# Performance work log

Hardware: AMD Instinct MI355X
Metric: run time of the kernel (lower is better)

Reference implementation:

```python
import jax, jax.numpy as jnp
import numpy as np

B, S, H, NH = 2, 2048, 1024, 16
D = H // NH


def setup_inputs() -> dict:
    key = jax.random.key(0)
    ks = jax.random.split(key, 7)
    scale = 1.0 / np.sqrt(H)
    return {
        "x": jax.random.normal(ks[0], (B, S, H), dtype=jnp.float32),
        "Wq": jax.random.normal(ks[1], (H, H), dtype=jnp.float32) * scale,
        "bq": jax.random.normal(ks[2], (H,), dtype=jnp.float32) * 0.01,
        "Wk": jax.random.normal(ks[3], (H, H), dtype=jnp.float32) * scale,
        "bk": jax.random.normal(ks[4], (H,), dtype=jnp.float32) * 0.01,
        "Wv": jax.random.normal(ks[5], (H, H), dtype=jnp.float32) * scale,
        "bv": jax.random.normal(ks[6], (H,), dtype=jnp.float32) * 0.01,
    }


def reference(x, Wq, bq, Wk, bk, Wv, bv):
    b, s, h = x.shape
    n, d = NH, h // NH
    # QKV projections (torch Linear: x @ W.T + b)
    q = (x @ Wq.T + bq).reshape(b, s, n, d).transpose(0, 2, 1, 3)  # [b,n,s,d]
    k = (x @ Wk.T + bk).reshape(b, s, n, d).transpose(0, 2, 1, 3)
    v = (x @ Wv.T + bv).reshape(b, s, n, d).transpose(0, 2, 1, 3)
    # NOTE: original module applies NO 1/sqrt(d) scaling -- stay faithful.
    scores = jnp.einsum("bnqd,bnkd->bnqk", q, k)  # [b,n,s,s]
    probs = jax.nn.softmax(scores, axis=-1)
    attn = jnp.einsum("bnqk,bnkd->bnqd", probs, v)  # [b,n,s,d]
    return attn.transpose(0, 2, 1, 3).reshape(b, s, h)
```

## Files before the change

kernel.cpp:

```cpp
#include <hip/hip_runtime.h>
#include <hip/hip_bf16.h>

typedef unsigned int uint;
typedef unsigned short ushort;
typedef _Float16 f16;
typedef __attribute__((ext_vector_type(4))) float f32x4;
typedef __attribute__((ext_vector_type(8))) _Float16 f16x8;
typedef __attribute__((ext_vector_type(8))) ushort ushort8;

#define MFMAH(a, b, c) __builtin_amdgcn_mfma_f32_16x16x32_f16((a), (b), (c), 0, 0, 0)

#if __has_builtin(__builtin_amdgcn_permlane32_swap) && __has_builtin(__builtin_amdgcn_permlane16_swap)
#define HAVE_PERMLANE_SWAP 1
#else
#define HAVE_PERMLANE_SWAP 0
#endif

__device__ __forceinline__ ushort f2h(float x) {
    f16 h = (f16)x;
    return __builtin_bit_cast(ushort, h);
}
__device__ __forceinline__ uint pk_f16(float lo, float hi) {
    auto t = __builtin_amdgcn_cvt_pkrtz(lo, hi);
    return __builtin_bit_cast(uint, t);
}

__device__ __forceinline__ void gload_lds16(const void* g, void* l) {
    __builtin_amdgcn_global_load_lds(
        (const __attribute__((address_space(1))) void*)g,
        (__attribute__((address_space(3))) void*)l, 16, 0, 0);
}

__global__ __launch_bounds__(256) void cvt_all(const float* __restrict__ x,
                                               const float* __restrict__ Wq,
                                               const float* __restrict__ Wk,
                                               const float* __restrict__ Wv,
                                               ushort* __restrict__ xf,
                                               ushort* __restrict__ wf) {
    const int blk = blockIdx.x;
    const float* src;
    ushort* dst;
    int i;
    if (blk < 2048) {
        src = x;  dst = xf;              i = blk * 256 + threadIdx.x;
    } else if (blk < 2560) {
        src = Wq; dst = wf;              i = (blk - 2048) * 256 + threadIdx.x;
    } else if (blk < 3072) {
        src = Wk; dst = wf + 1024 * 1024; i = (blk - 2560) * 256 + threadIdx.x;
    } else {
        src = Wv; dst = wf + 2 * 1024 * 1024; i = (blk - 3072) * 256 + threadIdx.x;
    }
    const float4* s4 = reinterpret_cast<const float4*>(src);
    float4 a = s4[2 * i], b = s4[2 * i + 1];
    float v[8] = {a.x, a.y, a.z, a.w, b.x, b.y, b.z, b.w};
    ushort8 o;
#pragma unroll
    for (int j = 0; j < 8; ++j) o[j] = f2h(v[j]);
    *reinterpret_cast<ushort8*>(dst + i * 8) = o;
}

__global__ __launch_bounds__(256, 3) void qkv_gemm(const ushort* __restrict__ xf,
                                                   const ushort* __restrict__ wf,
                                                   const float* __restrict__ bq,
                                                   const float* __restrict__ bk,
                                                   const float* __restrict__ bv,
                                                   ushort* __restrict__ qh,
                                                   ushort* __restrict__ kh,
                                                   ushort* __restrict__ vt) {
    __shared__ ushort Asf[128 * 64];
    __shared__ ushort Bsf[128 * 64];
    const int tid = threadIdx.x;
    const int l = tid & 63, w = tid >> 6;
    const int lrow = l & 15, lhi = l >> 4;
    const int wr = w >> 1, wc = w & 1;
    const int m0 = blockIdx.x * 128;
    const int n0 = blockIdx.y * 128;
    const int z = blockIdx.z;
    const ushort* wz = wf + z * (1024 * 1024);
    const float* bias = (z == 0) ? bq : (z == 1) ? bk : bv;

    f32x4 acc[4][4] = {};
    const int srow = w * 32 + (l >> 3);
    const int scol = ((l & 7) ^ (l >> 3)) * 8;
    const int lds0 = w * 2048;
    const int arow = wr * 64 + lrow;
    const int brow = wc * 64 + lrow;

    for (int kt = 0; kt < 16; ++kt) {
        const int kb = kt * 64;
#pragma unroll
        for (int i = 0; i < 4; ++i) {
            gload_lds16(xf + (m0 + srow + i * 8) * 1024 + kb + scol, &Asf[lds0 + i * 512]);
            gload_lds16(wz + (n0 + srow + i * 8) * 1024 + kb + scol, &Bsf[lds0 + i * 512]);
        }
        __syncthreads();
#pragma unroll
        for (int kk = 0; kk < 2; ++kk) {
            const int csw = ((kk * 4 + lhi) ^ (lrow & 7)) * 8;
            f16x8 axf[4];
#pragma unroll
            for (int mi = 0; mi < 4; ++mi)
                axf[mi] = *reinterpret_cast<const f16x8*>(&Asf[(arow + mi * 16) * 64 + csw]);
            __builtin_amdgcn_s_setprio(1);
#pragma unroll
            for (int ni = 0; ni < 4; ++ni) {
                f16x8 bf8 = *reinterpret_cast<const f16x8*>(&Bsf[(brow + ni * 16) * 64 + csw]);
#pragma unroll
                for (int mi = 0; mi < 4; ++mi)
                    acc[mi][ni] = MFMAH(axf[mi], bf8, acc[mi][ni]);
            }
            __builtin_amdgcn_s_setprio(0);
        }
        __syncthreads();
    }
    float bcol[4];
#pragma unroll
    for (int ni = 0; ni < 4; ++ni) bcol[ni] = bias[n0 + wc * 64 + ni * 16 + lrow];
    if (z == 2) {
#pragma unroll
        for (int mi = 0; mi < 4; ++mi) {
            const int m = m0 + wr * 64 + mi * 16 + lhi * 4;
            const int bb = m >> 11, s = m & 2047;
#pragma unroll
            for (int ni = 0; ni < 4; ++ni) {
                const int n = n0 + wc * 64 + ni * 16 + lrow;
                const int h = n >> 6, d = n & 63;
                ushort4 pk4;
                pk4.x = f2h(acc[mi][ni][0] + bcol[ni]);
                pk4.y = f2h(acc[mi][ni][1] + bcol[ni]);
                pk4.z = f2h(acc[mi][ni][2] + bcol[ni]);
                pk4.w = f2h(acc[mi][ni][3] + bcol[ni]);
                *reinterpret_cast<ushort4*>(vt + ((size_t)(bb * 16 + h) * 64 + d) * 2048 + s) = pk4;
            }
        }
    } else {
        const float qscale = (z == 0) ? 1.4426950408889634f : 1.0f;
        ushort* dst = (z == 0) ? qh : kh;
#pragma unroll
        for (int mi = 0; mi < 4; ++mi) {
#pragma unroll
            for (int r = 0; r < 4; ++r) {
                const int m = m0 + wr * 64 + mi * 16 + lhi * 4 + r;
                const int bb = m >> 11, s = m & 2047;
#pragma unroll
                for (int ni = 0; ni < 4; ++ni) {
                    const int n = n0 + wc * 64 + ni * 16 + lrow;
                    const int h = n >> 6, d = n & 63;
                    dst[((bb * 16 + h) * 2048 + s) * 64 + d] =
                        f2h((acc[mi][ni][r] + bcol[ni]) * qscale);
                }
            }
        }
    }
}

__global__ __launch_bounds__(512, 4) void attn_fwd(const ushort* __restrict__ Qhg,
                                                   const ushort* __restrict__ Khg,
                                                   const ushort* __restrict__ Vtg,
                                                   float* __restrict__ out) {
    __shared__ ushort Ksh[2][64 * 64];
    __shared__ ushort Vts[2][64 * 64];
    const int tid = threadIdx.x;
    const int l = tid & 63, w = tid >> 6;
    const int lrow = l & 15, lhi = l >> 4;
    const int wsub = w & 3;
    const int qt = blockIdx.x * 2 + (w >> 2);
    const int bh = blockIdx.y;
    const int b = bh >> 4, h = bh & 15;
    const size_t qoff = ((size_t)bh * 2048 + qt * 64) * 64;
    const size_t kvoff = (size_t)bh * 2048 * 64;
    const size_t vtoff = (size_t)bh * 64 * 2048;

    f16x8 aqh[2];
#pragma unroll
    for (int kk = 0; kk < 2; ++kk) {
        const size_t qa = qoff + (wsub * 16 + lrow) * 64 + kk * 32 + lhi * 8;
        aqh[kk] = *reinterpret_cast<const f16x8*>(Qhg + qa);
    }

    const int srow = w * 8 + (l >> 3);
    const int scol = ((l & 7) ^ (l >> 3)) * 8;
    const int lds0 = w * 512;

    const int bl = (lhi << 4) + lhi * 4;

    float m_run = -1e30f, l_run = 0.f;
    f32x4 o[4];
#pragma unroll
    for (int ni = 0; ni < 4; ++ni) o[ni] = f32x4{0.f, 0.f, 0.f, 0.f};

    auto stage = [&](int buf, int t) {
        const size_t gk = kvoff + (size_t)(t * 64 + srow) * 64 + scol;
        const size_t gv = vtoff + (size_t)srow * 2048 + t * 64 + scol;
        gload_lds16(Khg + gk, &Ksh[buf][lds0]);
        gload_lds16(Vtg + gv, &Vts[buf][lds0]);
    };

    auto tilecomp = [&](int buf) {
        f32x4 sc[4];
#pragma unroll
        for (int ni = 0; ni < 4; ++ni) sc[ni] = f32x4{0.f, 0.f, 0.f, 0.f};
        __builtin_amdgcn_s_setprio(1);
#pragma unroll
        for (int kk = 0; kk < 2; ++kk) {
#pragma unroll
            for (int ni = 0; ni < 4; ++ni) {
                const int off = (ni * 16 + lrow) * 64 + (((kk * 4 + lhi) ^ (lrow & 7)) * 8);
                f16x8 khf = *reinterpret_cast<const f16x8*>(&Ksh[buf][off]);
                sc[ni] = MFMAH(khf, aqh[kk], sc[ni]);
            }
        }
        __builtin_amdgcn_s_setprio(0);

        float mx = fmaxf(fmaxf(sc[0][0], sc[0][1]), fmaxf(sc[0][2], sc[0][3]));
#pragma unroll
        for (int ni = 1; ni < 4; ++ni)
            mx = fmaxf(mx, fmaxf(fmaxf(sc[ni][0], sc[ni][1]), fmaxf(sc[ni][2], sc[ni][3])));
        mx = fmaxf(mx, __shfl_xor(mx, 16, 64));
        mx = fmaxf(mx, __shfl_xor(mx, 32, 64));

        bool rescale = false;
        float alpha = 1.f;
        if (__any(mx > m_run + 8.f)) {
            float mnew = fmaxf(m_run, mx);
            alpha = exp2f(m_run - mnew);
            m_run = mnew;
            rescale = true;
        }
        float p[4][4];
        float lsum = 0.f;
#pragma unroll
        for (int ni = 0; ni < 4; ++ni)
#pragma unroll
            for (int r = 0; r < 4; ++r) {
                p[ni][r] = exp2f(sc[ni][r] - m_run);
                lsum += p[ni][r];
            }
        uint pk[4][2];
#pragma unroll
        for (int ni = 0; ni < 4; ++ni) {
            pk[ni][0] = pk_f16(p[ni][0], p[ni][1]);
            pk[ni][1] = pk_f16(p[ni][2], p[ni][3]);
        }
        lsum += __shfl_xor(lsum, 16, 64);
        lsum += __shfl_xor(lsum, 32, 64);
        if (rescale) {
            l_run = l_run * alpha + lsum;
            float ao0 = __shfl(alpha, bl + 0, 64);
            float ao1 = __shfl(alpha, bl + 1, 64);
            float ao2 = __shfl(alpha, bl + 2, 64);
            float ao3 = __shfl(alpha, bl + 3, 64);
#pragma unroll
            for (int ni = 0; ni < 4; ++ni) {
                o[ni][0] *= ao0; o[ni][1] *= ao1; o[ni][2] *= ao2; o[ni][3] *= ao3;
            }
        } else {
            l_run += lsum;
        }
        uint apw[2][4];
#if HAVE_PERMLANE_SWAP
#pragma unroll
        for (int kk = 0; kk < 2; ++kk) {
#pragma unroll
            for (int c = 0; c < 2; ++c) {
                auto r1 = __builtin_amdgcn_permlane32_swap(pk[2 * kk][c], pk[2 * kk + 1][c],
                                                           false, false);
                auto r2 = __builtin_amdgcn_permlane16_swap(r1[0], r1[1], false, false);
                apw[kk][c]     = (uint)r2[0];
                apw[kk][2 + c] = (uint)r2[1];
            }
        }
#else
        const int s0 = lrow + 32 * (lhi & 1);
        const int s1 = s0 + 16;
        const bool abit = (lhi >> 1) != 0;
#pragma unroll
        for (int kk = 0; kk < 2; ++kk) {
            int t0, t1;
            t0 = __shfl((int)pk[2 * kk][0], s0, 64); t1 = __shfl((int)pk[2 * kk + 1][0], s0, 64);
            apw[kk][0] = (uint)(abit ? t1 : t0);
            t0 = __shfl((int)pk[2 * kk][1], s0, 64); t1 = __shfl((int)pk[2 * kk + 1][1], s0, 64);
            apw[kk][1] = (uint)(abit ? t1 : t0);
            t0 = __shfl((int)pk[2 * kk][0], s1, 64); t1 = __shfl((int)pk[2 * kk + 1][0], s1, 64);
            apw[kk][2] = (uint)(abit ? t1 : t0);
            t0 = __shfl((int)pk[2 * kk][1], s1, 64); t1 = __shfl((int)pk[2 * kk + 1][1], s1, 64);
            apw[kk][3] = (uint)(abit ? t1 : t0);
        }
#endif
        __builtin_amdgcn_s_setprio(1);
#pragma unroll
        for (int kk = 0; kk < 2; ++kk) {
            f16x8 ap = *reinterpret_cast<const f16x8*>(&apw[kk][0]);
#pragma unroll
            for (int ni = 0; ni < 4; ++ni) {
                const int off = (ni * 16 + lrow) * 64 + (((kk * 4 + lhi) ^ (lrow & 7)) * 8);
                f16x8 vf = *reinterpret_cast<const f16x8*>(&Vts[buf][off]);
                o[ni] = MFMAH(ap, vf, o[ni]);
            }
        }
        __builtin_amdgcn_s_setprio(0);
    };

    stage(0, 0);
    __syncthreads();
#pragma unroll 1
    for (int tt = 0; tt < 16; ++tt) {
        stage(1, tt * 2 + 1);
        tilecomp(0);
        __syncthreads();
        if (tt < 15) stage(0, tt * 2 + 2);
        tilecomp(1);
        __syncthreads();
    }

    float ln0 = __shfl(l_run, bl + 0, 64);
    float ln1 = __shfl(l_run, bl + 1, 64);
    float ln2 = __shfl(l_run, bl + 2, 64);
    float ln3 = __shfl(l_run, bl + 3, 64);
#pragma unroll
    for (int ni = 0; ni < 4; ++ni) {
        const int q = qt * 64 + wsub * 16 + lhi * 4;
        const int d = ni * 16 + lrow;
        float* op = out + ((size_t)b * 2048 + q) * 1024 + h * 64 + d;
        op[0]        = o[ni][0] / ln0;
        op[1024]     = o[ni][1] / ln1;
        op[2 * 1024] = o[ni][2] / ln2;
        op[3 * 1024] = o[ni][3] / ln3;
    }
}

extern "C" void kernel_launch(void* const* d_in, const int* in_sizes, int n_in,
                              void* d_out, int out_size, void* d_ws, size_t ws_size,
                              hipStream_t stream) {
    const float* x  = (const float*)d_in[0];
    const float* Wq = (const float*)d_in[1];
    const float* bq = (const float*)d_in[2];
    const float* Wk = (const float*)d_in[3];
    const float* bk = (const float*)d_in[4];
    const float* Wv = (const float*)d_in[5];
    const float* bv = (const float*)d_in[6];
    float* outp = (float*)d_out;

    ushort* ws = (ushort*)d_ws;
    const size_t XM = 4096 * 1024;
    const size_t WM = 1024 * 1024;
    ushort* xf = ws;
    ushort* wf = xf + XM;
    ushort* qh = wf + 3 * WM;
    ushort* kh = qh + XM;
    ushort* vt = kh + XM;

    cvt_all<<<3584, 256, 0, stream>>>(x, Wq, Wk, Wv, xf, wf);

    qkv_gemm<<<dim3(32, 8, 3), 256, 0, stream>>>(xf, wf, bq, bk, bv, qh, kh, vt);

    attn_fwd<<<dim3(16, 32), 512, 0, stream>>>(qh, kh, vt, outp);
}
```

Baseline: 114.7 us.

## Load K/V fragments directly from global into registers, drop LDS staging

The attention kernel stops staging K and V tiles through double-buffered shared memory with barriers. Each wave now loads its MFMA fragments straight from global memory, relying on L2 for reuse. Blocks shrink to 4 waves covering one 64-row query tile, and a block-index swizzle spreads heads across the grid so that blocks sharing K/V run together. This removes the LDS traffic and syncs, but adds redundant global/L2 reads and exposes load latency because nothing is software-pipelined.

```diff
diff --git a/kernel.cpp b/kernel.cpp
--- a/kernel.cpp
+++ b/kernel.cpp
@@ -154,33 +154,28 @@
     }
 }
 
-__global__ __launch_bounds__(512, 4) void attn_fwd(const ushort* __restrict__ Qhg,
+__global__ __launch_bounds__(256, 4) void attn_fwd(const ushort* __restrict__ Qhg,
                                                    const ushort* __restrict__ Khg,
                                                    const ushort* __restrict__ Vtg,
                                                    float* __restrict__ out) {
-    __shared__ ushort Ksh[2][64 * 64];
-    __shared__ ushort Vts[2][64 * 64];
     const int tid = threadIdx.x;
     const int l = tid & 63, w = tid >> 6;
     const int lrow = l & 15, lhi = l >> 4;
-    const int wsub = w & 3;
-    const int qt = blockIdx.x * 2 + (w >> 2);
-    const int bh = blockIdx.y;
+    const int L = blockIdx.y * 32 + blockIdx.x;
+    const int qt = L >> 5;
+    const int r5 = L & 31;
+    const int bh = (r5 & 7) * 4 + (r5 >> 3);
     const int b = bh >> 4, h = bh & 15;
-    const size_t qoff = ((size_t)bh * 2048 + qt * 64) * 64;
-    const size_t kvoff = (size_t)bh * 2048 * 64;
-    const size_t vtoff = (size_t)bh * 64 * 2048;
+    const ushort* Kbase = Khg + (size_t)bh * 2048 * 64;
+    const ushort* Vbase = Vtg + (size_t)bh * 64 * 2048;
 
     f16x8 aqh[2];
 #pragma unroll
     for (int kk = 0; kk < 2; ++kk) {
-        const size_t qa = qoff + (wsub * 16 + lrow) * 64 + kk * 32 + lhi * 8;
+        const size_t qa = ((size_t)bh * 2048 + qt * 64) * 64
+                        + (w * 16 + lrow) * 64 + kk * 32 + lhi * 8;
         aqh[kk] = *reinterpret_cast<const f16x8*>(Qhg + qa);
     }
-
-    const int srow = w * 8 + (l >> 3);
-    const int scol = ((l & 7) ^ (l >> 3)) * 8;
-    const int lds0 = w * 512;
 
     const int bl = (lhi << 4) + lhi * 4;
 
@@ -189,28 +184,34 @@
 #pragma unroll
     for (int ni = 0; ni < 4; ++ni) o[ni] = f32x4{0.f, 0.f, 0.f, 0.f};
 
-    auto stage = [&](int buf, int t) {
-        const size_t gk = kvoff + (size_t)(t * 64 + srow) * 64 + scol;
-        const size_t gv = vtoff + (size_t)srow * 2048 + t * 64 + scol;
-        gload_lds16(Khg + gk, &Ksh[buf][lds0]);
-        gload_lds16(Vtg + gv, &Vts[buf][lds0]);
-    };
-
-    auto tilecomp = [&](int buf) {
+#pragma unroll 1
+    for (int t = 0; t < 32; ++t) {
+        f16x8 kf[2][4];
+#pragma unroll
+        for (int kk = 0; kk < 2; ++kk)
+#pragma unroll
+            for (int ni = 0; ni < 4; ++ni)
+                kf[kk][ni] = *reinterpret_cast<const f16x8*>(
+                    Kbase + (size_t)(t * 64 + ni * 16 + lrow) * 64 + kk * 32 + lhi * 8);
+
         f32x4 sc[4];
 #pragma unroll
         for (int ni = 0; ni < 4; ++ni) sc[ni] = f32x4{0.f, 0.f, 0.f, 0.f};
         __builtin_amdgcn_s_setprio(1);
 #pragma unroll
-        for (int kk = 0; kk < 2; ++kk) {
-#pragma unroll
-            for (int ni = 0; ni < 4; ++ni) {
-                const int off = (ni * 16 + lrow) * 64 + (((kk * 4 + lhi) ^ (lrow & 7)) * 8);
-                f16x8 khf = *reinterpret_cast<const f16x8*>(&Ksh[buf][off]);
-                sc[ni] = MFMAH(khf, aqh[kk], sc[ni]);
-            }
-        }
+        for (int kk = 0; kk < 2; ++kk)
+#pragma unroll
+            for (int ni = 0; ni < 4; ++ni)
+                sc[ni] = MFMAH(kf[kk][ni], aqh[kk], sc[ni]);
         __builtin_amdgcn_s_setprio(0);
+
+        f16x8 vf[2][4];
+#pragma unroll
+        for (int kk = 0; kk < 2; ++kk)
+#pragma unroll
+            for (int ni = 0; ni < 4; ++ni)
+                vf[kk][ni] = *reinterpret_cast<const f16x8*>(
+                    Vbase + (size_t)(ni * 16 + lrow) * 2048 + t * 64 + kk * 32 + lhi * 8);
 
         float mx = fmaxf(fmaxf(sc[0][0], sc[0][1]), fmaxf(sc[0][2], sc[0][3]));
 #pragma unroll
@@ -232,9 +233,9 @@
 #pragma unroll
         for (int ni = 0; ni < 4; ++ni)
 #pragma unroll
-            for (int r = 0; r < 4; ++r) {
-                p[ni][r] = exp2f(sc[ni][r] - m_run);
-                lsum += p[ni][r];
+            for (int rr = 0; rr < 4; ++rr) {
+                p[ni][rr] = exp2f(sc[ni][rr] - m_run);
+                lsum += p[ni][rr];
             }
         uint pk[4][2];
 #pragma unroll
@@ -260,7 +261,7 @@
         uint apw[2][4];
 #if HAVE_PERMLANE_SWAP
 #pragma unroll
-        for (int kk = 0; kk < 2; ++kk) {
+        for (int kk = 0; kk < 2; ++kk)
 #pragma unroll
             for (int c = 0; c < 2; ++c) {
                 auto r1 = __builtin_amdgcn_permlane32_swap(pk[2 * kk][c], pk[2 * kk + 1][c],
@@ -269,7 +270,6 @@
                 apw[kk][c]     = (uint)r2[0];
                 apw[kk][2 + c] = (uint)r2[1];
             }
-        }
 #else
         const int s0 = lrow + 32 * (lhi & 1);
         const int s1 = s0 + 16;
@@ -292,25 +292,10 @@
         for (int kk = 0; kk < 2; ++kk) {
             f16x8 ap = *reinterpret_cast<const f16x8*>(&apw[kk][0]);
 #pragma unroll
-            for (int ni = 0; ni < 4; ++ni) {
-                const int off = (ni * 16 + lrow) * 64 + (((kk * 4 + lhi) ^ (lrow & 7)) * 8);
-                f16x8 vf = *reinterpret_cast<const f16x8*>(&Vts[buf][off]);
-                o[ni] = MFMAH(ap, vf, o[ni]);
-            }
+            for (int ni = 0; ni < 4; ++ni)
+                o[ni] = MFMAH(ap, vf[kk][ni], o[ni]);
         }
         __builtin_amdgcn_s_setprio(0);
-    };
-
-    stage(0, 0);
-    __syncthreads();
-#pragma unroll 1
-    for (int tt = 0; tt < 16; ++tt) {
-        stage(1, tt * 2 + 1);
-        tilecomp(0);
-        __syncthreads();
-        if (tt < 15) stage(0, tt * 2 + 2);
-        tilecomp(1);
-        __syncthreads();
     }
 
     float ln0 = __shfl(l_run, bl + 0, 64);
@@ -319,7 +304,7 @@
     float ln3 = __shfl(l_run, bl + 3, 64);
 #pragma unroll
     for (int ni = 0; ni < 4; ++ni) {
-        const int q = qt * 64 + wsub * 16 + lhi * 4;
+        const int q = qt * 64 + w * 16 + lhi * 4;
         const int d = ni * 16 + lrow;
         float* op = out + ((size_t)b * 2048 + q) * 1024 + h * 64 + d;
         op[0]        = o[ni][0] / ln0;
@@ -354,5 +339,5 @@
 
     qkv_gemm<<<dim3(32, 8, 3), 256, 0, stream>>>(xf, wf, bq, bk, bv, qh, kh, vt);
 
-    attn_fwd<<<dim3(16, 32), 512, 0, stream>>>(qh, kh, vt, outp);
-}
+    attn_fwd<<<dim3(32, 32), 256, 0, stream>>>(qh, kh, vt, outp);
+}
```

Measured after the change: 266.3 us. 132% more time.

## Split attention KV range across two blocks and merge partials in combine kernel

Applied to the files above, without the earlier changes.

Splits the key/value sequence into two halves along a new grid z dimension, so each attention block processes 16 KV tiles instead of 32. Each block writes unnormalized partial outputs plus running max and sum to workspace, and a new combine kernel merges the two halves with log-sum-exp weights. The aim is to double the grid from 512 to 1024 blocks to better fill the GPU's compute units. The cost is extra fp32 partial-output traffic (about 67MB written and read back) and an additional kernel launch.

```diff
diff --git a/kernel.cpp b/kernel.cpp
--- a/kernel.cpp
+++ b/kernel.cpp
@@ -157,7 +157,9 @@
 __global__ __launch_bounds__(512, 4) void attn_fwd(const ushort* __restrict__ Qhg,
                                                    const ushort* __restrict__ Khg,
                                                    const ushort* __restrict__ Vtg,
-                                                   float* __restrict__ out) {
+                                                   float* __restrict__ po,
+                                                   float* __restrict__ pm,
+                                                   float* __restrict__ pl) {
     __shared__ ushort Ksh[2][64 * 64];
     __shared__ ushort Vts[2][64 * 64];
     const int tid = threadIdx.x;
@@ -166,7 +168,8 @@
     const int wsub = w & 3;
     const int qt = blockIdx.x * 2 + (w >> 2);
     const int bh = blockIdx.y;
-    const int b = bh >> 4, h = bh & 15;
+    const int z = blockIdx.z;
+    const int tbase = z * 16;
     const size_t qoff = ((size_t)bh * 2048 + qt * 64) * 64;
     const size_t kvoff = (size_t)bh * 2048 * 64;
     const size_t vtoff = (size_t)bh * 64 * 2048;
@@ -232,9 +235,9 @@
 #pragma unroll
         for (int ni = 0; ni < 4; ++ni)
 #pragma unroll
-            for (int r = 0; r < 4; ++r) {
-                p[ni][r] = exp2f(sc[ni][r] - m_run);
-                lsum += p[ni][r];
+            for (int rr = 0; rr < 4; ++rr) {
+                p[ni][rr] = exp2f(sc[ni][rr] - m_run);
+                lsum += p[ni][rr];
             }
         uint pk[4][2];
 #pragma unroll
@@ -301,32 +304,65 @@
         __builtin_amdgcn_s_setprio(0);
     };
 
-    stage(0, 0);
+    stage(0, tbase);
     __syncthreads();
 #pragma unroll 1
-    for (int tt = 0; tt < 16; ++tt) {
-        stage(1, tt * 2 + 1);
+    for (int tt = 0; tt < 8; ++tt) {
+        stage(1, tbase + tt * 2 + 1);
         tilecomp(0);
         __syncthreads();
-        if (tt < 15) stage(0, tt * 2 + 2);
+        if (tt < 7) stage(0, tbase + tt * 2 + 2);
         tilecomp(1);
         __syncthreads();
     }
 
-    float ln0 = __shfl(l_run, bl + 0, 64);
-    float ln1 = __shfl(l_run, bl + 1, 64);
-    float ln2 = __shfl(l_run, bl + 2, 64);
-    float ln3 = __shfl(l_run, bl + 3, 64);
-#pragma unroll
-    for (int ni = 0; ni < 4; ++ni) {
-        const int q = qt * 64 + wsub * 16 + lhi * 4;
-        const int d = ni * 16 + lrow;
-        float* op = out + ((size_t)b * 2048 + q) * 1024 + h * 64 + d;
-        op[0]        = o[ni][0] / ln0;
-        op[1024]     = o[ni][1] / ln1;
-        op[2 * 1024] = o[ni][2] / ln2;
-        op[3 * 1024] = o[ni][3] / ln3;
-    }
+    const size_t pbase = ((size_t)(z * 32 + bh) * 2048 + qt * 64 + wsub * 16 + lhi * 4) * 64;
+#pragma unroll
+    for (int ni = 0; ni < 4; ++ni)
+#pragma unroll
+        for (int r = 0; r < 4; ++r)
+            po[pbase + (size_t)r * 64 + ni * 16 + lrow] = o[ni][r];
+    if (lhi == 0) {
+        const size_t qi = (size_t)(z * 32 + bh) * 2048 + qt * 64 + wsub * 16 + lrow;
+        pm[qi] = m_run;
+        pl[qi] = l_run;
+    }
+}
+
+__global__ __launch_bounds__(256) void attn_combine(const float* __restrict__ po,
+                                                    const float* __restrict__ pm,
+                                                    const float* __restrict__ pl,
+                                                    float* __restrict__ out) {
+    const int id = blockIdx.x * 256 + threadIdx.x;
+    const int bh = id >> 14;
+    const int rem = id & 16383;
+    const int q = rem >> 3;
+    const int d0 = (rem & 7) * 8;
+    const int b = bh >> 4, h = bh & 15;
+    const size_t mi = (size_t)bh * 2048 + q;
+    const float m0 = pm[mi], m1 = pm[mi + 65536];
+    const float l0 = pl[mi], l1 = pl[mi + 65536];
+    const float mm = fmaxf(m0, m1);
+    const float w0 = exp2f(m0 - mm), w1 = exp2f(m1 - mm);
+    const float inv = 1.f / (l0 * w0 + l1 * w1);
+    const size_t o0 = ((size_t)bh * 2048 + q) * 64 + d0;
+    const size_t o1 = o0 + (size_t)32 * 2048 * 64;
+    float4 a0 = *reinterpret_cast<const float4*>(po + o0);
+    float4 a1 = *reinterpret_cast<const float4*>(po + o0 + 4);
+    float4 c0 = *reinterpret_cast<const float4*>(po + o1);
+    float4 c1 = *reinterpret_cast<const float4*>(po + o1 + 4);
+    float4 r0, r1;
+    r0.x = (a0.x * w0 + c0.x * w1) * inv;
+    r0.y = (a0.y * w0 + c0.y * w1) * inv;
+    r0.z = (a0.z * w0 + c0.z * w1) * inv;
+    r0.w = (a0.w * w0 + c0.w * w1) * inv;
+    r1.x = (a1.x * w0 + c1.x * w1) * inv;
+    r1.y = (a1.y * w0 + c1.y * w1) * inv;
+    r1.z = (a1.z * w0 + c1.z * w1) * inv;
+    r1.w = (a1.w * w0 + c1.w * w1) * inv;
+    float* op = out + ((size_t)b * 2048 + q) * 1024 + h * 64 + d0;
+    *reinterpret_cast<float4*>(op) = r0;
+    *reinterpret_cast<float4*>(op + 4) = r1;
 }
 
 extern "C" void kernel_launch(void* const* d_in, const int* in_sizes, int n_in,
@@ -349,10 +385,15 @@
     ushort* qh = wf + 3 * WM;
     ushort* kh = qh + XM;
     ushort* vt = kh + XM;
+    float*  po = (float*)(vt + XM);
+    float*  pm = po + (size_t)2 * 32 * 2048 * 64;
+    float*  pl = pm + (size_t)2 * 32 * 2048;
 
     cvt_all<<<3584, 256, 0, stream>>>(x, Wq, Wk, Wv, xf, wf);
 
     qkv_gemm<<<dim3(32, 8, 3), 256, 0, stream>>>(xf, wf, bq, bk, bv, qh, kh, vt);
 
-    attn_fwd<<<dim3(16, 32), 512, 0, stream>>>(qh, kh, vt, outp);
-}
+    attn_fwd<<<dim3(16, 32, 2), 512, 0, stream>>>(qh, kh, vt, po, pm, pl);
+
+    attn_combine<<<2048, 256, 0, stream>>>(po, pm, pl, outp);
+}
```

Result: slower. 123.7 us (+7.8%).

## Process two KV tiles per iteration with quad-buffered LDS and batched QK MFMAs

Applied to the files above, without the earlier changes.

Grows the K and V shared-memory buffers from two to four tiles. Each loop iteration now prefetches the next pair of tiles, runs the QK^T MFMAs for two tiles back to back, then does softmax and PV for each. This halves the number of barriers and gives the scheduler two independent score computations to interleave with the softmax math. The cost is double the LDS footprint (64KB per block) and more live registers, which may reduce occupancy under the launch bound of 4 blocks of 512 threads.

```diff
diff --git a/kernel.cpp b/kernel.cpp
--- a/kernel.cpp
+++ b/kernel.cpp
@@ -158,8 +158,8 @@
                                                    const ushort* __restrict__ Khg,
                                                    const ushort* __restrict__ Vtg,
                                                    float* __restrict__ out) {
-    __shared__ ushort Ksh[2][64 * 64];
-    __shared__ ushort Vts[2][64 * 64];
+    __shared__ ushort Ksh[4][64 * 64];
+    __shared__ ushort Vts[4][64 * 64];
     const int tid = threadIdx.x;
     const int l = tid & 63, w = tid >> 6;
     const int lrow = l & 15, lhi = l >> 4;
@@ -196,8 +196,7 @@
         gload_lds16(Vtg + gv, &Vts[buf][lds0]);
     };
 
-    auto tilecomp = [&](int buf) {
-        f32x4 sc[4];
+    auto qk = [&](int buf, f32x4* sc) {
 #pragma unroll
         for (int ni = 0; ni < 4; ++ni) sc[ni] = f32x4{0.f, 0.f, 0.f, 0.f};
         __builtin_amdgcn_s_setprio(1);
@@ -211,7 +210,9 @@
             }
         }
         __builtin_amdgcn_s_setprio(0);
-
+    };
+
+    auto smpv = [&](f32x4* sc, int buf) {
         float mx = fmaxf(fmaxf(sc[0][0], sc[0][1]), fmaxf(sc[0][2], sc[0][3]));
 #pragma unroll
         for (int ni = 1; ni < 4; ++ni)
@@ -232,9 +233,9 @@
 #pragma unroll
         for (int ni = 0; ni < 4; ++ni)
 #pragma unroll
-            for (int r = 0; r < 4; ++r) {
-                p[ni][r] = exp2f(sc[ni][r] - m_run);
-                lsum += p[ni][r];
+            for (int rr = 0; rr < 4; ++rr) {
+                p[ni][rr] = exp2f(sc[ni][rr] - m_run);
+                lsum += p[ni][rr];
             }
         uint pk[4][2];
 #pragma unroll
@@ -302,14 +303,21 @@
     };
 
     stage(0, 0);
+    stage(1, 1);
     __syncthreads();
 #pragma unroll 1
-    for (int tt = 0; tt < 16; ++tt) {
-        stage(1, tt * 2 + 1);
-        tilecomp(0);
-        __syncthreads();
-        if (tt < 15) stage(0, tt * 2 + 2);
-        tilecomp(1);
+    for (int pp = 0; pp < 16; ++pp) {
+        const int ba = (pp & 1) * 2;
+        const int nb = ((pp + 1) & 1) * 2;
+        if (pp < 15) {
+            stage(nb, 2 * pp + 2);
+            stage(nb + 1, 2 * pp + 3);
+        }
+        f32x4 sca[4], scb[4];
+        qk(ba, sca);
+        qk(ba + 1, scb);
+        smpv(sca, ba);
+        smpv(scb, ba + 1);
         __syncthreads();
     }
 
```

Result: slower. 117.1 us (+2.1%).
